# Performance work log

Hardware: AMD Instinct MI355X
Metric: run time of the kernel (lower is better)

The kernel has to match this reference:

```python
import jax, jax.numpy as jnp
import numpy as np

L, B, T, E, H, V = 6, 4, 1024, 768, 12, 32000
FF = 4 * E


def setup_inputs() -> dict:
    key = jax.random.key(0)
    ks = jax.random.split(key, 16)
    n = lambda k, shape: jax.random.normal(k, shape, jnp.float32) * 0.02
    return {
        "idx": jax.random.randint(ks[0], (B, T), 0, V),
        "targets": jax.random.randint(ks[1], (B, T), 0, V),
        "tok_emb": n(ks[2], (V, E)),
        "pos_emb": n(ks[3], (T, E)),  # block_size == T
        "Wq": n(ks[4], (L, E, E)),
        "Wk": n(ks[5], (L, E, E)),
        "Wv": n(ks[6], (L, E, E)),
        "Wp": n(ks[7], (L, E, E)),
        "bp": jnp.zeros((L, E), jnp.float32),
        "W1": n(ks[8], (L, E, FF)),
        "b1": jnp.zeros((L, FF), jnp.float32),
        "W2": n(ks[9], (L, FF, E)),
        "b2": jnp.zeros((L, E), jnp.float32),
        "ln1_g": jnp.ones((L, E), jnp.float32),
        "ln1_b": jnp.zeros((L, E), jnp.float32),
        "ln2_g": jnp.ones((L, E), jnp.float32),
        "ln2_b": jnp.zeros((L, E), jnp.float32),
        "lnf_g": jnp.ones((E,), jnp.float32),
        "lnf_b": jnp.zeros((E,), jnp.float32),
        "Wlm": n(ks[10], (E, V)),
        "blm": jnp.zeros((V,), jnp.float32),
    }


def _ln(x, g, b):
    m = jnp.mean(x, -1, keepdims=True)
    v = jnp.var(x, -1, keepdims=True)
    return (x - m) * jax.lax.rsqrt(v + 1e-5) * g + b


def _attn(x, wq, wk, wv, wp, pb):
    b, t, e = x.shape
    hs = e // H
    q = (x @ wq).reshape(b, t, H, hs).transpose(0, 2, 1, 3)
    k = (x @ wk).reshape(b, t, H, hs).transpose(0, 2, 1, 3)
    v = (x @ wv).reshape(b, t, H, hs).transpose(0, 2, 1, 3)
    s = jnp.einsum('bhqd,bhkd->bhqk', q, k) * (hs ** -0.5)
    mask = jnp.tril(jnp.ones((t, t), bool))
    s = jnp.where(mask, s, -jnp.inf)
    p = jax.nn.softmax(s, axis=-1)  # dropout = identity at eval
    o = jnp.einsum('bhqk,bhkd->bhqd', p, v).transpose(0, 2, 1, 3).reshape(b, t, e)
    return o @ wp + pb


def reference(idx, targets, tok_emb, pos_emb, Wq, Wk, Wv, Wp, bp, W1, b1, W2, b2,
              ln1_g, ln1_b, ln2_g, ln2_b, lnf_g, lnf_b, Wlm, blm):
    x = tok_emb[idx] + pos_emb[:idx.shape[1]]

    def step(x, p):
        wq, wk, wv, wp, pb, w1, pb1, w2, pb2, g1, bb1, g2, bb2 = p
        x = x + _attn(_ln(x, g1, bb1), wq, wk, wv, wp, pb)
        h = _ln(x, g2, bb2)
        x = x + (jax.nn.relu(h @ w1 + pb1) @ w2 + pb2)
        return x, None

    x, _ = jax.lax.scan(step, x, (Wq, Wk, Wv, Wp, bp, W1, b1, W2, b2,
                                  ln1_g, ln1_b, ln2_g, ln2_b))
    x = _ln(x, lnf_g, lnf_b)
    logits = x @ Wlm + blm
    logp = jax.nn.log_softmax(logits, axis=-1)
    loss = -jnp.mean(jnp.take_along_axis(logp, targets[..., None], axis=-1))
    return logits, loss
```

## Files before the change

### kernel.cpp

```cpp
#include <hip/hip_runtime.h>
#include <hip/hip_bf16.h>
#include <math.h>

#define LAYERS 6
#define BB 4
#define TT 1024
#define EE 768
#define HH 12
#define HS 64
#define VV 32000
#define FFD 3072
#define MROWS (BB * TT)
#define QS (3 * EE)
#define KVB 64
#define QBLK 128
#define NPART (VV / 256)

typedef __attribute__((ext_vector_type(8))) short bf16x8_t;
typedef __attribute__((ext_vector_type(4))) float f32x4_t;

__device__ __forceinline__ float wave_sum(float v) {
#pragma unroll
    for (int o = 32; o > 0; o >>= 1) v += __shfl_xor(v, o);
    return v;
}
__device__ __forceinline__ float wave_max(float v) {
#pragma unroll
    for (int o = 32; o > 0; o >>= 1) v = fmaxf(v, __shfl_xor(v, o));
    return v;
}
__device__ __forceinline__ float block_sum256(float v, float* red) {
    v = wave_sum(v);
    int tid = threadIdx.x;
    if ((tid & 63) == 0) red[tid >> 6] = v;
    __syncthreads();
    float r = red[0] + red[1] + red[2] + red[3];
    __syncthreads();
    return r;
}
__device__ __forceinline__ float block_max256(float v, float* red) {
    v = wave_max(v);
    int tid = threadIdx.x;
    if ((tid & 63) == 0) red[tid >> 6] = v;
    __syncthreads();
    float r = fmaxf(fmaxf(red[0], red[1]), fmaxf(red[2], red[3]));
    __syncthreads();
    return r;
}

__device__ __forceinline__ void gload_lds16(const void* g, void* l) {
    __builtin_amdgcn_global_load_lds((const __attribute__((address_space(1))) void*)g,
                                     (__attribute__((address_space(3))) void*)l, 16, 0, 0);
}

__device__ __forceinline__ unsigned pk2bf(float lo, float hi) {
    __hip_bfloat162 h2 = __float22bfloat162_rn(make_float2(lo, hi));
    return *reinterpret_cast<unsigned*>(&h2);
}

__global__ __launch_bounds__(256) void embed4_k(const int* __restrict__ idx,
                                                const float* __restrict__ tok,
                                                const float* __restrict__ pos,
                                                float* __restrict__ x) {
    int row = blockIdx.x * 4 + (threadIdx.x >> 6);
    int lane = threadIdx.x & 63;
    int t = row & (TT - 1);
    int token = idx[row];
    const float4* te = (const float4*)(tok + (size_t)token * EE);
    const float4* pe = (const float4*)(pos + (size_t)t * EE);
    float4* xr = (float4*)(x + (size_t)row * EE);
#pragma unroll
    for (int j = 0; j < 3; ++j) {
        int i = j * 64 + lane;
        float4 a = te[i], b = pe[i];
        xr[i] = make_float4(a.x + b.x, a.y + b.y, a.z + b.z, a.w + b.w);
    }
}

__global__ __launch_bounds__(256) void ln4_k(const float* __restrict__ x,
                                             const float* __restrict__ g,
                                             const float* __restrict__ b,
                                             __hip_bfloat16* __restrict__ out) {
    int row = blockIdx.x * 4 + (threadIdx.x >> 6);
    int lane = threadIdx.x & 63;
    const float4* xr = (const float4*)(x + (size_t)row * EE);
    float4 v[3];
    float s = 0.f;
#pragma unroll
    for (int j = 0; j < 3; ++j) {
        v[j] = xr[j * 64 + lane];
        s += v[j].x + v[j].y + v[j].z + v[j].w;
    }
    s = wave_sum(s);
    float m = s * (1.0f / EE);
    float vs = 0.f;
#pragma unroll
    for (int j = 0; j < 3; ++j) {
        float d0 = v[j].x - m, d1 = v[j].y - m, d2 = v[j].z - m, d3 = v[j].w - m;
        vs += d0 * d0 + d1 * d1 + d2 * d2 + d3 * d3;
    }
    vs = wave_sum(vs);
    float rstd = rsqrtf(vs * (1.0f / EE) + 1e-5f);
    const float4* g4 = (const float4*)g;
    const float4* b4 = (const float4*)b;
    uint2* orow = (uint2*)(out + (size_t)row * EE);
#pragma unroll
    for (int j = 0; j < 3; ++j) {
        int i = j * 64 + lane;
        float4 gg = g4[i], bb = b4[i];
        float n0 = (v[j].x - m) * rstd * gg.x + bb.x;
        float n1 = (v[j].y - m) * rstd * gg.y + bb.y;
        float n2 = (v[j].z - m) * rstd * gg.z + bb.z;
        float n3 = (v[j].w - m) * rstd * gg.w + bb.w;
        orow[i] = make_uint2(pk2bf(n0, n1), pk2bf(n2, n3));
    }
}

__global__ __launch_bounds__(256) void tconv_b_k(const float* __restrict__ W,
                                                 __hip_bfloat16* __restrict__ WT,
                                                 int R, int C,
                                                 size_t wstride, size_t tstride) {
    __shared__ float t[32][33];
    const float* Wl = W + (size_t)blockIdx.z * wstride;
    __hip_bfloat16* Tl = WT + (size_t)blockIdx.z * tstride;
    int c0 = blockIdx.x * 32, r0 = blockIdx.y * 32;
    int tx = threadIdx.x & 31, ty = threadIdx.x >> 5;
#pragma unroll
    for (int i = 0; i < 4; ++i)
        t[ty + 8 * i][tx] = Wl[(size_t)(r0 + ty + 8 * i) * C + c0 + tx];
    __syncthreads();
#pragma unroll
    for (int i = 0; i < 4; ++i)
        Tl[(size_t)(c0 + ty + 8 * i) * R + r0 + tx] = __float2bfloat16(t[tx][ty + 8 * i]);
}

template <bool BIAS, bool RELU, bool ACCUM, bool OBF16, int MI>
__global__ __launch_bounds__(256) void mgemm_k(const __hip_bfloat16* __restrict__ A,
                                               const __hip_bfloat16* __restrict__ BT,
                                               const float* __restrict__ bias,
                                               void* __restrict__ Cv,
                                               int M, int N, int K, int ntn) {
    __shared__ __align__(16) short As[MI * 32 * 32];
    __shared__ __align__(16) short Bs[128 * 32];

    int nwg = gridDim.x;
    int bid = blockIdx.x;
    int cpx = nwg >> 3;
    int swz = (bid & 7) * cpx + (bid >> 3);
    int tm = swz / ntn, tn = swz - tm * ntn;
    int m0 = tm * (MI * 32), n0 = tn * 128;

    int tid = threadIdx.x;
    int lane = tid & 63;
    int wave = tid >> 6;
    int wr = wave >> 1, wc = wave & 1;

    f32x4_t acc[MI][4];
#pragma unroll
    for (int i = 0; i < MI; ++i)
#pragma unroll
        for (int j = 0; j < 4; ++j)
#pragma unroll
            for (int r = 0; r < 4; ++r) acc[i][j][r] = 0.f;

    const short* Ag = (const short*)A;
    const short* Bg = (const short*)BT;
    const int arow0 = tid >> 2;
    const int arow1 = (tid + 256) >> 2;
    const int acol = (tid & 3) * 8;

    const int fr = lane & 15;
    const int kg = (lane >> 4) * 8;

    for (int k0 = 0; k0 < K; k0 += 32) {
        gload_lds16(Ag + (size_t)(m0 + arow0) * K + k0 + acol, &As[tid * 8]);
        if (MI == 4)
            gload_lds16(Ag + (size_t)(m0 + arow1) * K + k0 + acol, &As[(tid + 256) * 8]);
        gload_lds16(Bg + (size_t)(n0 + arow0) * K + k0 + acol, &Bs[tid * 8]);
        gload_lds16(Bg + (size_t)(n0 + arow1) * K + k0 + acol, &Bs[(tid + 256) * 8]);
        __syncthreads();

        bf16x8_t af[MI], bq[4];
#pragma unroll
        for (int mi = 0; mi < MI; ++mi)
            af[mi] = *(const bf16x8_t*)&As[(wr * (MI * 16) + mi * 16 + fr) * 32 + kg];
#pragma unroll
        for (int ni = 0; ni < 4; ++ni)
            bq[ni] = *(const bf16x8_t*)&Bs[(wc * 64 + ni * 16 + fr) * 32 + kg];
#pragma unroll
        for (int mi = 0; mi < MI; ++mi)
#pragma unroll
            for (int ni = 0; ni < 4; ++ni)
                acc[mi][ni] = __builtin_amdgcn_mfma_f32_16x16x32_bf16(af[mi], bq[ni], acc[mi][ni], 0, 0, 0);
        __syncthreads();
    }

    float bvec[4];
    if (BIAS) {
#pragma unroll
        for (int ni = 0; ni < 4; ++ni) bvec[ni] = bias[n0 + wc * 64 + ni * 16 + fr];
    }
    const int rbase = m0 + wr * (MI * 16) + (lane >> 4) * 4;
    const int cbase = n0 + wc * 64 + fr;
#pragma unroll
    for (int mi = 0; mi < MI; ++mi) {
#pragma unroll
        for (int ni = 0; ni < 4; ++ni) {
#pragma unroll
            for (int r = 0; r < 4; ++r) {
                int row = rbase + mi * 16 + r;
                int col = cbase + ni * 16;
                float v = acc[mi][ni][r];
                if (BIAS) v += bvec[ni];
                if (RELU) v = fmaxf(v, 0.f);
                size_t off = (size_t)row * N + col;
                if (OBF16) {
                    ((__hip_bfloat16*)Cv)[off] = __float2bfloat16(v);
                } else {
                    float* Cf = (float*)Cv;
                    if (ACCUM) Cf[off] += v; else Cf[off] = v;
                }
            }
        }
    }
}

__device__ __forceinline__ bf16x8_t ldsrd256(const short* base, int row, int colb) {
    return *(const bf16x8_t*)((const char*)base + ((row << 7) + (colb ^ ((row & 7) << 4))));
}

template <bool BIAS, bool RELU, bool OBF16, bool LSE>
__global__ __launch_bounds__(512, 2) void mgemm256_k(const __hip_bfloat16* __restrict__ A,
                                                     const __hip_bfloat16* __restrict__ BT,
                                                     const float* __restrict__ bias,
                                                     void* __restrict__ Cv,
                                                     int M, int N, int K,
                                                     int ntn, int npart,
                                                     float2* __restrict__ partials) {
    __shared__ __align__(16) short lds[2][2][2][8192];

    const int nwg = gridDim.x;
    const int bid = blockIdx.x;
    const int cpx = nwg >> 3;
    const int swz = (bid & 7) * cpx + (bid >> 3);
    const int tm = swz / ntn, tn = swz - tm * ntn;
    const int m0 = tm * 256, n0 = tn * 256;

    const int tid = threadIdx.x;
    const int lane = tid & 63;
    const int wave = tid >> 6;
    const int wm = wave >> 2;
    const int wn = wave & 3;
    const int fr = lane & 15;
    const int hi4 = lane >> 4;

    const short* Ag = (const short*)A;
    const short* Bg = (const short*)BT;
    const int nt = K >> 6;

    auto stage_half = [&](const short* g, int grow0, int k0, short* lbase) {
#pragma unroll
        for (int sub = 0; sub < 2; ++sub) {
            int d = sub * 8192 + tid * 16;
            int row = d >> 7;
            int cb = d & 127;
            int col = (cb ^ ((row & 7) << 4)) >> 1;
            gload_lds16(g + (size_t)(grow0 + row) * K + k0 + col, (char*)lbase + d);
        }
    };

    f32x4_t acc[2][2][4][2];
#pragma unroll
    for (int ah = 0; ah < 2; ++ah)
#pragma unroll
        for (int s = 0; s < 2; ++s)
#pragma unroll
            for (int mi = 0; mi < 4; ++mi)
#pragma unroll
                for (int ni = 0; ni < 2; ++ni)
#pragma unroll
                    for (int r = 0; r < 4; ++r) acc[ah][s][mi][ni][r] = 0.f;

    stage_half(Ag, m0 + 0,   0,  &lds[0][0][0][0]);
    stage_half(Bg, n0 + 0,   0,  &lds[0][1][0][0]);
    stage_half(Ag, m0 + 128, 0,  &lds[0][0][1][0]);
    stage_half(Bg, n0 + 128, 0,  &lds[0][1][1][0]);
    stage_half(Ag, m0 + 0,   64, &lds[1][0][0][0]);
    stage_half(Bg, n0 + 0,   64, &lds[1][1][0][0]);
    asm volatile("s_waitcnt vmcnt(4)" ::: "memory");
    __builtin_amdgcn_s_barrier();

    for (int t = 0; t < nt; ++t) {
        const int c = t & 1, o = c ^ 1;
        bf16x8_t a[4][2];
#pragma unroll
        for (int p = 0; p < 4; ++p) {
            const int ah = p >> 1, s = p & 1;
            if (s == 0) {
#pragma unroll
                for (int mi = 0; mi < 4; ++mi)
#pragma unroll
                    for (int kk = 0; kk < 2; ++kk)
                        a[mi][kk] = ldsrd256(&lds[c][0][ah][0],
                                             wm * 64 + mi * 16 + fr, kk * 64 + hi4 * 16);
            }
            bf16x8_t b[2][2];
#pragma unroll
            for (int ni = 0; ni < 2; ++ni)
#pragma unroll
                for (int kk = 0; kk < 2; ++kk)
                    b[ni][kk] = ldsrd256(&lds[c][1][s][0],
                                         wn * 32 + ni * 16 + fr, kk * 64 + hi4 * 16);
            if (p == 0 && t + 1 < nt) stage_half(Ag, m0 + 128, (t + 1) * 64, &lds[o][0][1][0]);
            if (p == 1 && t + 1 < nt) stage_half(Bg, n0 + 128, (t + 1) * 64, &lds[o][1][1][0]);
            if (p == 2 && t + 2 < nt) stage_half(Ag, m0 + 0,   (t + 2) * 64, &lds[c][0][0][0]);
            if (p == 3 && t + 2 < nt) stage_half(Bg, n0 + 0,   (t + 2) * 64, &lds[c][1][0][0]);
            if (p == 3) {
                if (t < nt - 2)       asm volatile("s_waitcnt vmcnt(4)" ::: "memory");
                else if (t == nt - 2) asm volatile("s_waitcnt vmcnt(0)" ::: "memory");
            }
            __builtin_amdgcn_s_barrier();
            asm volatile("s_waitcnt lgkmcnt(0)" ::: "memory");
            __builtin_amdgcn_sched_barrier(0);
            __builtin_amdgcn_s_setprio(1);
#pragma unroll
            for (int mi = 0; mi < 4; ++mi)
#pragma unroll
                for (int ni = 0; ni < 2; ++ni)
#pragma unroll
                    for (int kk = 0; kk < 2; ++kk)
                        acc[ah][s][mi][ni] = __builtin_amdgcn_mfma_f32_16x16x32_bf16(
                            a[mi][kk], b[ni][kk], acc[ah][s][mi][ni], 0, 0, 0);
            __builtin_amdgcn_s_setprio(0);
            __builtin_amdgcn_s_barrier();
        }
    }

    float bv[2][2];
    if (BIAS) {
#pragma unroll
        for (int s = 0; s < 2; ++s)
#pragma unroll
            for (int ni = 0; ni < 2; ++ni)
                bv[s][ni] = bias[n0 + s * 128 + wn * 32 + ni * 16 + fr];
    }
    float2* red = (float2*)&lds[0][0][0][0];
#pragma unroll
    for (int ah = 0; ah < 2; ++ah) {
#pragma unroll
        for (int mi = 0; mi < 4; ++mi) {
#pragma unroll
            for (int r = 0; r < 4; ++r) {
                const int rb = ah * 128 + wm * 64 + mi * 16 + hi4 * 4 + r;
                const size_t grow = (size_t)(m0 + rb);
                float v[2][2];
#pragma unroll
                for (int s = 0; s < 2; ++s)
#pragma unroll
                    for (int ni = 0; ni < 2; ++ni) {
                        float vv = acc[ah][s][mi][ni][r];
                        if (BIAS) vv += bv[s][ni];
                        if (RELU) vv = fmaxf(vv, 0.f);
                        v[s][ni] = vv;
                        size_t off = grow * N + n0 + s * 128 + wn * 32 + ni * 16 + fr;
                        if (OBF16) ((__hip_bfloat16*)Cv)[off] = __float2bfloat16(vv);
                        else       ((float*)Cv)[off] = vv;
                    }
                if (LSE) {
                    float mx = fmaxf(fmaxf(v[0][0], v[0][1]), fmaxf(v[1][0], v[1][1]));
#pragma unroll
                    for (int off2 = 1; off2 < 16; off2 <<= 1) mx = fmaxf(mx, __shfl_xor(mx, off2));
                    float sm = 0.f;
#pragma unroll
                    for (int s = 0; s < 2; ++s)
#pragma unroll
                        for (int ni = 0; ni < 2; ++ni) sm += __expf(v[s][ni] - mx);
#pragma unroll
                    for (int off2 = 1; off2 < 16; off2 <<= 1) sm += __shfl_xor(sm, off2);
                    if (fr == 0) red[rb * 4 + wn] = make_float2(mx, sm);
                }
            }
        }
    }
    if (LSE) {
        __syncthreads();
        if (tid < 256) {
            float2 p0 = red[tid * 4 + 0], p1 = red[tid * 4 + 1];
            float2 p2 = red[tid * 4 + 2], p3 = red[tid * 4 + 3];
            float M2 = fmaxf(fmaxf(p0.x, p1.x), fmaxf(p2.x, p3.x));
            float L2 = p0.y * __expf(p0.x - M2) + p1.y * __expf(p1.x - M2) +
                       p2.y * __expf(p2.x - M2) + p3.y * __expf(p3.x - M2);
            partials[(size_t)(m0 + tid) * npart + tn] = make_float2(M2, L2);
        }
    }
}

__global__ __launch_bounds__(256) void fattn_k(const __hip_bfloat16* __restrict__ qkv,
                                               __hip_bfloat16* __restrict__ o) {
    __shared__ short Ks[KVB * HS];
    __shared__ short Vt[HS * KVB];
    __shared__ short Pl[4 * 32 * KVB];

    const int bh = blockIdx.x;
    const int hh = bh % HH;
    const int bI = bh / HH;
    const int qt = (TT / QBLK - 1) - blockIdx.y;
    const int q0 = qt * QBLK;

    const int tid = threadIdx.x;
    const int lane = tid & 63;
    const int wave = tid >> 6;
    const int fr = lane & 15;
    const int hi4 = lane >> 4;

    const size_t rowbase = (size_t)bI * TT;
    const int wq0 = q0 + wave * 32;

    bf16x8_t qf[2][2];
#pragma unroll
    for (int mi = 0; mi < 2; ++mi)
#pragma unroll
        for (int kc = 0; kc < 2; ++kc) {
            const short* src = (const short*)qkv +
                (rowbase + wq0 + mi * 16 + fr) * QS + hh * HS + kc * 32 + hi4 * 8;
            bf16x8_t v = *(const bf16x8_t*)src;
#pragma unroll
            for (int e = 0; e < 8; ++e) {
                float f = __uint_as_float(((unsigned)(unsigned short)v[e]) << 16) * 0.125f;
                v[e] = (short)(__float_as_uint(f) >> 16);
            }
            qf[mi][kc] = v;
        }

    f32x4_t oa[2][4];
    float m_r[2], l_r[2];
#pragma unroll
    for (int mi = 0; mi < 2; ++mi) {
        m_r[mi] = -INFINITY;
        l_r[mi] = 0.f;
#pragma unroll
        for (int nd = 0; nd < 4; ++nd)
#pragma unroll
            for (int r = 0; r < 4; ++r) oa[mi][nd][r] = 0.f;
    }

    const int skey = tid >> 2;
    const int sd0 = (tid & 3) * 16;
    const int niter = 2 * (qt + 1);

    uint4 ka, kb2, va, vb2;
    {
        const short* kg = (const short*)qkv + (rowbase + skey) * QS + EE + hh * HS + sd0;
        ka = *(const uint4*)kg; kb2 = *(const uint4*)(kg + 8);
        const short* vg = (const short*)qkv + (rowbase + skey) * QS + 2 * EE + hh * HS + sd0;
        va = *(const uint4*)vg; vb2 = *(const uint4*)(vg + 8);
    }

    for (int it = 0; it < niter; ++it) {
        __syncthreads();
        {
            const int rs = (skey & 7) << 4;
            char* kbp = (char*)Ks;
            *(uint4*)(kbp + ((skey * 128 + sd0 * 2) ^ rs)) = ka;
            *(uint4*)(kbp + ((skey * 128 + sd0 * 2 + 16) ^ rs)) = kb2;

            char* vbp = (char*)Vt;
            const short* vs0 = (const short*)&va;
#pragma unroll
            for (int e = 0; e < 8; ++e) {
                int dd = sd0 + e;
                *(short*)(vbp + ((dd * 128 + skey * 2) ^ ((dd & 7) << 4))) = vs0[e];
            }
            const short* vs1 = (const short*)&vb2;
#pragma unroll
            for (int e = 0; e < 8; ++e) {
                int dd = sd0 + 8 + e;
                *(short*)(vbp + ((dd * 128 + skey * 2) ^ ((dd & 7) << 4))) = vs1[e];
            }
        }
        __syncthreads();

        if (it + 1 < niter) {
            const int kvn = (it + 1) * KVB;
            const short* kg = (const short*)qkv + (rowbase + kvn + skey) * QS + EE + hh * HS + sd0;
            ka = *(const uint4*)kg; kb2 = *(const uint4*)(kg + 8);
            const short* vg = (const short*)qkv + (rowbase + kvn + skey) * QS + 2 * EE + hh * HS + sd0;
            va = *(const uint4*)vg; vb2 = *(const uint4*)(vg + 8);
        }

        const int kv0 = it * KVB;

        f32x4_t sa[2][4];
#pragma unroll
        for (int mi = 0; mi < 2; ++mi)
#pragma unroll
            for (int ni = 0; ni < 4; ++ni)
#pragma unroll
                for (int r = 0; r < 4; ++r) sa[mi][ni][r] = 0.f;
        __builtin_amdgcn_s_setprio(1);
#pragma unroll
        for (int kc = 0; kc < 2; ++kc) {
            bf16x8_t kf[4];
#pragma unroll
            for (int ni = 0; ni < 4; ++ni) {
                int krow = ni * 16 + fr;
                kf[ni] = *(const bf16x8_t*)((char*)Ks +
                    ((krow * 128 + (kc * 32 + hi4 * 8) * 2) ^ ((krow & 7) << 4)));
            }
#pragma unroll
            for (int mi = 0; mi < 2; ++mi)
#pragma unroll
                for (int ni = 0; ni < 4; ++ni)
                    sa[mi][ni] = __builtin_amdgcn_mfma_f32_16x16x32_bf16(kf[ni], qf[mi][kc], sa[mi][ni], 0, 0, 0);
        }
        __builtin_amdgcn_s_setprio(0);

        if (kv0 + KVB - 1 > wq0) {
#pragma unroll
            for (int mi = 0; mi < 2; ++mi) {
                int qrow = wq0 + mi * 16 + fr;
#pragma unroll
                for (int ni = 0; ni < 4; ++ni)
#pragma unroll
                    for (int r = 0; r < 4; ++r) {
                        int key = kv0 + ni * 16 + hi4 * 4 + r;
                        if (key > qrow) sa[mi][ni][r] = -1e30f;
                    }
            }
        }

        char* Pw = (char*)Pl + wave * 4096;
#pragma unroll
        for (int mi = 0; mi < 2; ++mi) {
            float mx = sa[mi][0][0];
#pragma unroll
            for (int ni = 0; ni < 4; ++ni)
#pragma unroll
                for (int r = 0; r < 4; ++r) mx = fmaxf(mx, sa[mi][ni][r]);
            mx = fmaxf(mx, __shfl_xor(mx, 16));
            mx = fmaxf(mx, __shfl_xor(mx, 32));
            if (!__all(mx <= m_r[mi] + 8.0f)) {
                float mnew = fmaxf(m_r[mi], mx);
                float al = __expf(m_r[mi] - mnew);
                m_r[mi] = mnew;
                l_r[mi] *= al;
#pragma unroll
                for (int r = 0; r < 4; ++r) {
                    float a_r = __shfl(al, hi4 * 4 + r);
#pragma unroll
                    for (int nd = 0; nd < 4; ++nd) oa[mi][nd][r] *= a_r;
                }
            }
            float ps = 0.f;
#pragma unroll
            for (int ni = 0; ni < 4; ++ni) {
#pragma unroll
                for (int r = 0; r < 4; ++r) {
                    float p = __expf(sa[mi][ni][r] - m_r[mi]);
                    sa[mi][ni][r] = p;
                    ps += p;
                }
                uint2 pw;
                pw.x = pk2bf(sa[mi][ni][0], sa[mi][ni][1]);
                pw.y = pk2bf(sa[mi][ni][2], sa[mi][ni][3]);
                int prow = mi * 16 + fr;
                int cb = ni * 32 + hi4 * 8;
                *(uint2*)(Pw + ((prow * 128 + cb) ^ ((prow & 7) << 4))) = pw;
            }
            ps += __shfl_xor(ps, 16);
            ps += __shfl_xor(ps, 32);
            l_r[mi] += ps;
        }

        __builtin_amdgcn_s_setprio(1);
#pragma unroll
        for (int kc = 0; kc < 2; ++kc) {
            bf16x8_t pf[2], vf[4];
#pragma unroll
            for (int mi = 0; mi < 2; ++mi) {
                int prow = mi * 16 + fr;
                pf[mi] = *(const bf16x8_t*)(Pw +
                    ((prow * 128 + (kc * 32 + hi4 * 8) * 2) ^ ((prow & 7) << 4)));
            }
#pragma unroll
            for (int nd = 0; nd < 4; ++nd) {
                int vrow = nd * 16 + fr;
                vf[nd] = *(const bf16x8_t*)((char*)Vt +
                    ((vrow * 128 + (kc * 32 + hi4 * 8) * 2) ^ ((vrow & 7) << 4)));
            }
#pragma unroll
            for (int mi = 0; mi < 2; ++mi)
#pragma unroll
                for (int nd = 0; nd < 4; ++nd)
                    oa[mi][nd] = __builtin_amdgcn_mfma_f32_16x16x32_bf16(pf[mi], vf[nd], oa[mi][nd], 0, 0, 0);
        }
        __builtin_amdgcn_s_setprio(0);
    }

#pragma unroll
    for (int mi = 0; mi < 2; ++mi)
#pragma unroll
        for (int r = 0; r < 4; ++r) {
            float lr = __shfl(l_r[mi], hi4 * 4 + r);
            float inv = 1.0f / lr;
            int row = wq0 + mi * 16 + hi4 * 4 + r;
            __hip_bfloat16* orow = o + (rowbase + row) * EE + hh * HS;
#pragma unroll
            for (int nd = 0; nd < 4; ++nd)
                orow[nd * 16 + fr] = __float2bfloat16(oa[mi][nd][r] * inv);
        }
}

__global__ __launch_bounds__(256) void rowloss2_k(const float2* __restrict__ partials,
                                                  const float* __restrict__ logits,
                                                  const int* __restrict__ targets,
                                                  float* __restrict__ rowloss, int ntn) {
    __shared__ float red[4];
    int row = blockIdx.x;
    int tid = threadIdx.x;
    float m = -INFINITY, l = 0.f;
    if (tid < ntn) {
        float2 p = partials[(size_t)row * ntn + tid];
        m = p.x; l = p.y;
    }
    float mg = block_max256(m, red);
    float s = (tid < ntn) ? l * __expf(m - mg) : 0.f;
    s = block_sum256(s, red);
    if (tid == 0)
        rowloss[row] = mg + logf(s) - logits[(size_t)row * VV + targets[row]];
}

__global__ __launch_bounds__(256) void loss_final_k(const float* __restrict__ rowloss,
                                                    float* __restrict__ out) {
    __shared__ float red[4];
    float s = 0.f;
    for (int i = threadIdx.x; i < MROWS; i += 256) s += rowloss[i];
    s = block_sum256(s, red);
    if (threadIdx.x == 0) out[0] = s * (1.0f / MROWS);
}

extern "C" void kernel_launch(void* const* d_in, const int* in_sizes, int n_in,
                              void* d_out, int out_size, void* d_ws, size_t ws_size,
                              hipStream_t stream) {
    const int* idx      = (const int*)d_in[0];
    const int* targets  = (const int*)d_in[1];
    const float* tok    = (const float*)d_in[2];
    const float* pos    = (const float*)d_in[3];
    const float* Wq     = (const float*)d_in[4];
    const float* Wk     = (const float*)d_in[5];
    const float* Wv     = (const float*)d_in[6];
    const float* Wp     = (const float*)d_in[7];
    const float* bp     = (const float*)d_in[8];
    const float* W1     = (const float*)d_in[9];
    const float* b1     = (const float*)d_in[10];
    const float* W2     = (const float*)d_in[11];
    const float* b2     = (const float*)d_in[12];
    const float* ln1_g  = (const float*)d_in[13];
    const float* ln1_b  = (const float*)d_in[14];
    const float* ln2_g  = (const float*)d_in[15];
    const float* ln2_b  = (const float*)d_in[16];
    const float* lnf_g  = (const float*)d_in[17];
    const float* lnf_b  = (const float*)d_in[18];
    const float* Wlm    = (const float*)d_in[19];
    const float* blm    = (const float*)d_in[20];

    float* out = (float*)d_out;

    char* w = (char*)d_ws;
    float* x = (float*)w;                             w += (size_t)MROWS * EE * 4;
    __hip_bfloat16* hbf = (__hip_bfloat16*)w;         w += (size_t)MROWS * EE * 2;
    __hip_bfloat16* qkv = (__hip_bfloat16*)w;         w += (size_t)MROWS * QS * 2;
    __hip_bfloat16* obf = (__hip_bfloat16*)w;         w += (size_t)MROWS * EE * 2;
    __hip_bfloat16* ff1 = (__hip_bfloat16*)w;         w += (size_t)MROWS * FFD * 2;
    float2* partials = (float2*)ff1;
    __hip_bfloat16* wlmT = (__hip_bfloat16*)w;        w += (size_t)VV * EE * 2;
    float* rowloss = (float*)w;                       w += (size_t)MROWS * 4 + 256;
    __hip_bfloat16* wbase = (__hip_bfloat16*)w;

    const size_t base_used = (size_t)(w - (char*)d_ws);
    const size_t per_layer_w = ((size_t)QS * EE + (size_t)EE * EE +
                                (size_t)FFD * EE + (size_t)EE * FFD) * 2;
    const bool hoist = ws_size >= base_used + per_layer_w * LAYERS;
    const int nlw = hoist ? LAYERS : 1;

    __hip_bfloat16* qkvwT = wbase;
    __hip_bfloat16* wpT   = qkvwT + (size_t)nlw * QS * EE;
    __hip_bfloat16* w1T   = wpT   + (size_t)nlw * EE * EE;
    __hip_bfloat16* w2T   = w1T   + (size_t)nlw * FFD * EE;

    dim3 blk(256);

    embed4_k<<<MROWS / 4, blk, 0, stream>>>(idx, tok, pos, x);

    if (hoist) {
        tconv_b_k<<<dim3(EE / 32, EE / 32, LAYERS), blk, 0, stream>>>(
            Wq, qkvwT, EE, EE, (size_t)EE * EE, (size_t)QS * EE);
        tconv_b_k<<<dim3(EE / 32, EE / 32, LAYERS), blk, 0, stream>>>(
            Wk, qkvwT + (size_t)EE * EE, EE, EE, (size_t)EE * EE, (size_t)QS * EE);
        tconv_b_k<<<dim3(EE / 32, EE / 32, LAYERS), blk, 0, stream>>>(
            Wv, qkvwT + (size_t)2 * EE * EE, EE, EE, (size_t)EE * EE, (size_t)QS * EE);
        tconv_b_k<<<dim3(EE / 32, EE / 32, LAYERS), blk, 0, stream>>>(
            Wp, wpT, EE, EE, (size_t)EE * EE, (size_t)EE * EE);
        tconv_b_k<<<dim3(FFD / 32, EE / 32, LAYERS), blk, 0, stream>>>(
            W1, w1T, EE, FFD, (size_t)EE * FFD, (size_t)FFD * EE);
        tconv_b_k<<<dim3(EE / 32, FFD / 32, LAYERS), blk, 0, stream>>>(
            W2, w2T, FFD, EE, (size_t)FFD * EE, (size_t)EE * FFD);
    }
    tconv_b_k<<<dim3(VV / 32, EE / 32, 1), blk, 0, stream>>>(Wlm, wlmT, EE, VV, 0, 0);

    for (int l = 0; l < LAYERS; ++l) {
        __hip_bfloat16* qkvwT_l = qkvwT + (hoist ? (size_t)l * QS * EE : 0);
        __hip_bfloat16* wpT_l   = wpT   + (hoist ? (size_t)l * EE * EE : 0);
        __hip_bfloat16* w1T_l   = w1T   + (hoist ? (size_t)l * FFD * EE : 0);
        __hip_bfloat16* w2T_l   = w2T   + (hoist ? (size_t)l * EE * FFD : 0);
        if (!hoist) {
            tconv_b_k<<<dim3(EE / 32, EE / 32, 1), blk, 0, stream>>>(
                Wq + (size_t)l * EE * EE, qkvwT_l, EE, EE, 0, 0);
            tconv_b_k<<<dim3(EE / 32, EE / 32, 1), blk, 0, stream>>>(
                Wk + (size_t)l * EE * EE, qkvwT_l + (size_t)EE * EE, EE, EE, 0, 0);
            tconv_b_k<<<dim3(EE / 32, EE / 32, 1), blk, 0, stream>>>(
                Wv + (size_t)l * EE * EE, qkvwT_l + (size_t)2 * EE * EE, EE, EE, 0, 0);
            tconv_b_k<<<dim3(EE / 32, EE / 32, 1), blk, 0, stream>>>(
                Wp + (size_t)l * EE * EE, wpT_l, EE, EE, 0, 0);
            tconv_b_k<<<dim3(FFD / 32, EE / 32, 1), blk, 0, stream>>>(
                W1 + (size_t)l * EE * FFD, w1T_l, EE, FFD, 0, 0);
            tconv_b_k<<<dim3(EE / 32, FFD / 32, 1), blk, 0, stream>>>(
                W2 + (size_t)l * FFD * EE, w2T_l, FFD, EE, 0, 0);
        }

        ln4_k<<<MROWS / 4, blk, 0, stream>>>(x, ln1_g + l * EE, ln1_b + l * EE, hbf);
        mgemm_k<false, false, false, true, 4><<<dim3((MROWS / 128) * (QS / 128)), blk, 0, stream>>>(
            hbf, qkvwT_l, nullptr, qkv, MROWS, QS, EE, QS / 128);
        fattn_k<<<dim3(BB * HH, TT / QBLK), blk, 0, stream>>>(qkv, obf);
        mgemm_k<true, false, true, false, 2><<<dim3((MROWS / 64) * (EE / 128)), blk, 0, stream>>>(
            obf, wpT_l, bp + l * EE, x, MROWS, EE, EE, EE / 128);
        ln4_k<<<MROWS / 4, blk, 0, stream>>>(x, ln2_g + l * EE, ln2_b + l * EE, hbf);
        mgemm_k<true, true, false, true, 4><<<dim3((MROWS / 128) * (FFD / 128)), blk, 0, stream>>>(
            hbf, w1T_l, b1 + l * FFD, ff1, MROWS, FFD, EE, FFD / 128);
        mgemm_k<true, false, true, false, 2><<<dim3((MROWS / 64) * (EE / 128)), blk, 0, stream>>>(
            ff1, w2T_l, b2 + l * EE, x, MROWS, EE, FFD, EE / 128);
    }

    ln4_k<<<MROWS / 4, blk, 0, stream>>>(x, lnf_g, lnf_b, hbf);
    mgemm256_k<true, false, false, true><<<dim3((MROWS / 256) * (VV / 256)), dim3(512), 0, stream>>>(
        hbf, wlmT, blm, out, MROWS, VV, EE, VV / 256, NPART, partials);

    rowloss2_k<<<MROWS, blk, 0, stream>>>(partials, out, targets, rowloss, NPART);
    loss_final_k<<<1, blk, 0, stream>>>(rowloss, out + (size_t)MROWS * VV);
}
```

Before: 1.602 ms.

## Pre-transpose V per head, reorder LM-head tile walk, shrink QKV GEMM tiles

Adds a small kernel that writes V transposed per (batch, head) into a new workspace buffer. Flash attention can then stage V into shared memory with two vector stores instead of sixteen scattered 2-byte stores per thread. The LM-head GEMM now walks tiles M-fastest within each N column, and the QKV projection uses 64-row tiles instead of 128-row tiles for more workgroups. The cost is one extra kernel launch per layer and an extra read and write of V, plus more workspace memory.

```diff
diff --git a/kernel.cpp b/kernel.cpp
--- a/kernel.cpp
+++ b/kernel.cpp
@@ -134,6 +134,24 @@
         Tl[(size_t)(c0 + ty + 8 * i) * R + r0 + tx] = __float2bfloat16(t[tx][ty + 8 * i]);
 }
 
+__global__ __launch_bounds__(256) void vtrans_k(const __hip_bfloat16* __restrict__ qkv,
+                                                __hip_bfloat16* __restrict__ vT) {
+    __shared__ short t[32][33];
+    const int z = blockIdx.z;
+    const int b = z / HH, h = z % HH;
+    const int t0 = blockIdx.x * 32, d0 = blockIdx.y * 32;
+    const int tx = threadIdx.x & 31, ty = threadIdx.x >> 5;
+    const short* src = (const short*)qkv;
+    short* dst = (short*)vT;
+#pragma unroll
+    for (int i = 0; i < 4; ++i)
+        t[ty + 8 * i][tx] = src[((size_t)(b * TT + t0 + ty + 8 * i)) * QS + 2 * EE + h * HS + d0 + tx];
+    __syncthreads();
+#pragma unroll
+    for (int i = 0; i < 4; ++i)
+        dst[((size_t)((b * HH + h) * HS + d0 + ty + 8 * i)) * TT + t0 + tx] = t[tx][ty + 8 * i];
+}
+
 template <bool BIAS, bool RELU, bool ACCUM, bool OBF16, int MI>
 __global__ __launch_bounds__(256) void mgemm_k(const __hip_bfloat16* __restrict__ A,
                                                const __hip_bfloat16* __restrict__ BT,
@@ -243,7 +261,8 @@
     const int bid = blockIdx.x;
     const int cpx = nwg >> 3;
     const int swz = (bid & 7) * cpx + (bid >> 3);
-    const int tm = swz / ntn, tn = swz - tm * ntn;
+    const int ntm = M >> 8;
+    const int tn = swz / ntm, tm = swz - tn * ntm;
     const int m0 = tm * 256, n0 = tn * 256;
 
     const int tid = threadIdx.x;
@@ -396,6 +415,7 @@
 }
 
 __global__ __launch_bounds__(256) void fattn_k(const __hip_bfloat16* __restrict__ qkv,
+                                               const __hip_bfloat16* __restrict__ vT,
                                                __hip_bfloat16* __restrict__ o) {
     __shared__ short Ks[KVB * HS];
     __shared__ short Vt[HS * KVB];
@@ -414,6 +434,7 @@
     const int hi4 = lane >> 4;
 
     const size_t rowbase = (size_t)bI * TT;
+    const short* vTbase = (const short*)vT + ((size_t)(bI * HH + hh) * HS) * TT;
     const int wq0 = q0 + wave * 32;
 
     bf16x8_t qf[2][2];
@@ -452,7 +473,7 @@
     {
         const short* kg = (const short*)qkv + (rowbase + skey) * QS + EE + hh * HS + sd0;
         ka = *(const uint4*)kg; kb2 = *(const uint4*)(kg + 8);
-        const short* vg = (const short*)qkv + (rowbase + skey) * QS + 2 * EE + hh * HS + sd0;
+        const short* vg = vTbase + (size_t)skey * TT + sd0;
         va = *(const uint4*)vg; vb2 = *(const uint4*)(vg + 8);
     }
 
@@ -465,18 +486,8 @@
             *(uint4*)(kbp + ((skey * 128 + sd0 * 2 + 16) ^ rs)) = kb2;
 
             char* vbp = (char*)Vt;
-            const short* vs0 = (const short*)&va;
-#pragma unroll
-            for (int e = 0; e < 8; ++e) {
-                int dd = sd0 + e;
-                *(short*)(vbp + ((dd * 128 + skey * 2) ^ ((dd & 7) << 4))) = vs0[e];
-            }
-            const short* vs1 = (const short*)&vb2;
-#pragma unroll
-            for (int e = 0; e < 8; ++e) {
-                int dd = sd0 + 8 + e;
-                *(short*)(vbp + ((dd * 128 + skey * 2) ^ ((dd & 7) << 4))) = vs1[e];
-            }
+            *(uint4*)(vbp + ((skey * 128 + sd0 * 2) ^ rs)) = va;
+            *(uint4*)(vbp + ((skey * 128 + sd0 * 2 + 16) ^ rs)) = vb2;
         }
         __syncthreads();
 
@@ -484,7 +495,7 @@
             const int kvn = (it + 1) * KVB;
             const short* kg = (const short*)qkv + (rowbase + kvn + skey) * QS + EE + hh * HS + sd0;
             ka = *(const uint4*)kg; kb2 = *(const uint4*)(kg + 8);
-            const short* vg = (const short*)qkv + (rowbase + kvn + skey) * QS + 2 * EE + hh * HS + sd0;
+            const short* vg = vTbase + (size_t)skey * TT + kvn + sd0;
             va = *(const uint4*)vg; vb2 = *(const uint4*)(vg + 8);
         }
 
@@ -671,6 +682,7 @@
     __hip_bfloat16* hbf = (__hip_bfloat16*)w;         w += (size_t)MROWS * EE * 2;
     __hip_bfloat16* qkv = (__hip_bfloat16*)w;         w += (size_t)MROWS * QS * 2;
     __hip_bfloat16* obf = (__hip_bfloat16*)w;         w += (size_t)MROWS * EE * 2;
+    __hip_bfloat16* vTb = (__hip_bfloat16*)w;         w += (size_t)BB * HH * HS * TT * 2;
     __hip_bfloat16* ff1 = (__hip_bfloat16*)w;         w += (size_t)MROWS * FFD * 2;
     float2* partials = (float2*)ff1;
     __hip_bfloat16* wlmT = (__hip_bfloat16*)w;        w += (size_t)VV * EE * 2;
@@ -729,9 +741,10 @@
         }
 
         ln4_k<<<MROWS / 4, blk, 0, stream>>>(x, ln1_g + l * EE, ln1_b + l * EE, hbf);
-        mgemm_k<false, false, false, true, 4><<<dim3((MROWS / 128) * (QS / 128)), blk, 0, stream>>>(
+        mgemm_k<false, false, false, true, 2><<<dim3((MROWS / 64) * (QS / 128)), blk, 0, stream>>>(
             hbf, qkvwT_l, nullptr, qkv, MROWS, QS, EE, QS / 128);
-        fattn_k<<<dim3(BB * HH, TT / QBLK), blk, 0, stream>>>(qkv, obf);
+        vtrans_k<<<dim3(TT / 32, HS / 32, BB * HH), blk, 0, stream>>>(qkv, vTb);
+        fattn_k<<<dim3(BB * HH, TT / QBLK), blk, 0, stream>>>(qkv, vTb, obf);
         mgemm_k<true, false, true, false, 2><<<dim3((MROWS / 64) * (EE / 128)), blk, 0, stream>>>(
             obf, wpT_l, bp + l * EE, x, MROWS, EE, EE, EE / 128);
         ln4_k<<<MROWS / 4, blk, 0, stream>>>(x, ln2_g + l * EE, ln2_b + l * EE, hbf);
```

Result: no change. 1.627 ms (+1.6%).
